# Kernel tuning notes

Measured on AMD Instinct MI355X. Metric: run time of the kernel, lower is better.

Reference implementation:

```python
import jax, jax.numpy as jnp
import numpy as np

NEG_INF = -1e30


def setup_inputs() -> dict:
    B, N, D = 512, 256, 256
    key = jax.random.key(0)
    ks = jax.random.split(key, 10)
    s = 1.0 / np.sqrt(D)
    return {
        "enc": jax.random.normal(ks[0], (B, N, D), dtype=jnp.float32),
        "init_token": jax.random.normal(ks[1], (D,), dtype=jnp.float32),
        "w_ih": jax.random.uniform(ks[2], (3 * D, D), minval=-s, maxval=s, dtype=jnp.float32),
        "w_hh": jax.random.uniform(ks[3], (3 * D, D), minval=-s, maxval=s, dtype=jnp.float32),
        "b_ih": jax.random.uniform(ks[4], (3 * D,), minval=-s, maxval=s, dtype=jnp.float32),
        "b_hh": jax.random.uniform(ks[5], (3 * D,), minval=-s, maxval=s, dtype=jnp.float32),
        "wq": jax.random.uniform(ks[6], (D, D), minval=-s, maxval=s, dtype=jnp.float32),
        "bq": jax.random.uniform(ks[7], (D,), minval=-s, maxval=s, dtype=jnp.float32),
        "wk": jax.random.uniform(ks[8], (D, D), minval=-s, maxval=s, dtype=jnp.float32),
        "bk": jax.random.uniform(ks[9], (D,), minval=-s, maxval=s, dtype=jnp.float32),
    }


def gru_cell(x, h, w_ih, w_hh, b_ih, b_hh):
    # torch.nn.GRUCell math; gates packed as [reset, update, new]
    gi = x @ w_ih.T + b_ih          # [B, 3D]
    gh = h @ w_hh.T + b_hh          # [B, 3D]
    D = h.shape[-1]
    i_r, i_z, i_n = gi[:, :D], gi[:, D:2 * D], gi[:, 2 * D:]
    h_r, h_z, h_n = gh[:, :D], gh[:, D:2 * D], gh[:, 2 * D:]
    r = jax.nn.sigmoid(i_r + h_r)
    z = jax.nn.sigmoid(i_z + h_z)
    n = jnp.tanh(i_n + r * h_n)
    return (1.0 - z) * n + z * h


def pointer_decode(enc, init_token, w_ih, w_hh, b_ih, b_hh, wq, bq, wk, bk):
    # Greedy decode (deterministic analogue of decode_type='greedy').
    B, N, D = enc.shape
    scale = 1.0 / np.sqrt(D)
    keys = enc @ wk.T + bk                         # [B, N, D]
    rows = jnp.arange(B)

    def step(carry, _):
        state, prev_embed, mask = carry
        state = gru_cell(prev_embed, state, w_ih, w_hh, b_ih, b_hh)   # [B, D]
        query = state @ wq.T + bq                                     # [B, D]
        logits = jnp.einsum('bd,bnd->bn', query, keys) * scale        # [B, N]
        logits = jnp.where(mask, logits, NEG_INF)
        logp = jax.nn.log_softmax(logits, axis=-1)                    # [B, N]
        probs = jnp.exp(logp)
        entropy = -jnp.sum(probs * jnp.where(mask, logp, 0.0), axis=-1)  # [B]
        idx = jnp.argmax(probs, axis=-1)                              # [B]
        step_logp = logp[rows, idx]                                   # [B]
        prev_embed = enc[rows, idx]                                   # [B, D]
        mask = mask.at[rows, idx].set(False)
        return (state, prev_embed, mask), (idx, step_logp, entropy)

    carry0 = (enc.mean(axis=1),
              jnp.broadcast_to(init_token, (B, D)),
              jnp.ones((B, N), dtype=bool))
    _, (tours, logps, ents) = jax.lax.scan(step, carry0, None, length=N)
    return tours.T, logps.T, ents.T  # each [B, N]


def reference(enc, init_token, w_ih, w_hh, b_ih, b_hh, wq, bq, wk, bk):
    return pointer_decode(enc, init_token, w_ih, w_hh, b_ih, b_hh, wq, bq, wk, bk)
```

## Files before the change

### kernel.cpp

```cpp
#include <hip/hip_runtime.h>

#define B_ 512
#define N_ 256
#define D_ 256
#define NEGINF (-1e30)
#define LN2_ 0.693147180559945309417232121458

#define PDX(c) ((c) + (((c) >> 6) << 1))

typedef float v4f __attribute__((ext_vector_type(4)));

__device__ __forceinline__ v4f ntload4(const v4f* p) {
  return __builtin_nontemporal_load(p);
}
__device__ __forceinline__ double ntload8(const double* p) {
  return __builtin_nontemporal_load(p);
}

__global__ void transpose_k(const float* __restrict__ in, float* __restrict__ out,
                            int R, int C) {
  __shared__ float tile[32][33];
  int rb = blockIdx.y * 32, cb = blockIdx.x * 32;
  int tx = threadIdx.x, ty = threadIdx.y;
  for (int i = ty; i < 32; i += 8) {
    int r = rb + i, c = cb + tx;
    if (r < R && c < C) tile[i][tx] = in[r * C + c];
  }
  __syncthreads();
  for (int i = ty; i < 32; i += 8) {
    int c = cb + i, r = rb + tx;
    if (r < R && c < C) out[c * R + r] = tile[tx][i];
  }
}

__global__ __launch_bounds__(256) void packW_k(const float* __restrict__ in,
                                               float* __restrict__ out) {
  int idx = blockIdx.x * 256 + threadIdx.x;
  int j = idx >> 6, c4 = idx & 63;
  int g = j >> 8, o = j & 255;
  int WV = o >> 5, S = c4 >> 5, k = c4 & 31, l = 2 * (o & 31) + S;
  ((v4f*)out)[((WV * 32 + k) * 3 + g) * 64 + l] = ((const v4f*)in)[idx];
}

__global__ __launch_bounds__(256) void wqk_k(const float* __restrict__ wk,
                                             const float* __restrict__ wq,
                                             const float* __restrict__ bq,
                                             double* __restrict__ WqkP,
                                             double* __restrict__ bqk) {
  int c = blockIdx.x, e = threadIdx.x;
  double acc = 0.0;
  for (int dd = 0; dd < 256; ++dd)
    acc += (double)wk[dd * 256 + c] * (double)wq[dd * 256 + e];
  int WV = c >> 5, l = 2 * (c & 31) + (e >> 7), k = (e & 127) >> 1, comp = e & 1;
  WqkP[(size_t)((WV * 64 + k) * 64 + l) * 2 + comp] = acc;
  if (e == 0) {
    double s = 0.0;
    for (int dd = 0; dd < 256; ++dd) s += (double)wk[dd * 256 + c] * (double)bq[dd];
    bqk[c] = s;
  }
}

__global__ __launch_bounds__(256) void encp_k(const float* __restrict__ enc,
                                              float* __restrict__ encP) {
  int b = blockIdx.y;
  int idx = blockIdx.x * 256 + threadIdx.x;
  int l = idx & 63, rest = idx >> 6;
  int k = rest & 31, WV = rest >> 5;
  int n = WV * 32 + (l >> 1), c4 = (l & 1) * 32 + k;
  ((v4f*)encP)[(size_t)b * 16384 + idx] =
      *(const v4f*)(enc + (size_t)b * 65536 + n * 256 + c4 * 4);
}

__global__ __launch_bounds__(768) void gi_k(const float* __restrict__ enc,
                                            const float* __restrict__ wihT,
                                            const float* __restrict__ b_ih,
                                            double* __restrict__ Gi) {
  int b = blockIdx.x, j = threadIdx.x;
  __shared__ float encS[32][256];
  const float* encB = enc + (size_t)b * 65536;
  double bias = (double)b_ih[j];
  for (int n0 = 0; n0 < 256; n0 += 32) {
    __syncthreads();
    for (int i = j; i < 2048; i += 768)
      ((float4*)encS)[i] = ((const float4*)(encB + n0 * 256))[i];
    __syncthreads();
    double acc[32];
#pragma unroll
    for (int jj = 0; jj < 32; ++jj) acc[jj] = bias;
    for (int c0 = 0; c0 < 256; c0 += 4) {
      double w0 = (double)wihT[(c0 + 0) * 768 + j];
      double w1 = (double)wihT[(c0 + 1) * 768 + j];
      double w2 = (double)wihT[(c0 + 2) * 768 + j];
      double w3 = (double)wihT[(c0 + 3) * 768 + j];
#pragma unroll
      for (int jj = 0; jj < 32; ++jj) {
        const float4 e = *(const float4*)&encS[jj][c0];
        acc[jj] += w0 * (double)e.x + w1 * (double)e.y + w2 * (double)e.z + w3 * (double)e.w;
      }
    }
#pragma unroll
    for (int jj = 0; jj < 32; ++jj)
      Gi[((size_t)b * 256 + n0 + jj) * 768 + j] = acc[jj];
  }
}

__global__ __launch_bounds__(768) void gi0_k(const float* __restrict__ w_ih,
                                             const float* __restrict__ b_ih,
                                             const float* __restrict__ init_token,
                                             double* __restrict__ gi0) {
  int j = threadIdx.x;
  __shared__ float xs[256];
  if (j < 256) xs[j] = init_token[j];
  __syncthreads();
  double acc = (double)b_ih[j];
  for (int c = 0; c < 256; ++c) acc += (double)w_ih[j * 256 + c] * (double)xs[c];
  gi0[j] = acc;
}

template <bool USE_GI>
__global__ __launch_bounds__(512, 4) void decode_k(
    const float* __restrict__ enc, const float* __restrict__ init_token,
    const float* __restrict__ b_ih, const float* __restrict__ b_hh,
    const float* __restrict__ wihP, const float* __restrict__ whhP,
    const double* __restrict__ WqkP, const double* __restrict__ bqk,
    const float* __restrict__ encP, const double* __restrict__ gi0,
    const double* __restrict__ Gi, float* __restrict__ out) {
  const int tid = threadIdx.x;
  const int WV = tid >> 6;
  const int LN = tid & 63;
  const int O = WV * 32 + (LN >> 1);
  const int S = LN & 1;
  const int b = blockIdx.x;
  const int OP = PDX(O);
  const int CB = S * 132;

  __shared__ alignas(16) double hS[2][264];
  __shared__ alignas(16) double xS[264];
  __shared__ alignas(16) double qs[264];
  __shared__ unsigned char maskS[N_];
  __shared__ double redA[8], redB[8], redC[8];
  __shared__ int redI[8];

  const float* encB = enc + (size_t)b * 65536;
  const v4f* eP = (const v4f*)encP + (size_t)b * 16384;
  const v4f* wh4 = (const v4f*)whhP;
  const v4f* wi4 = (const v4f*)wihP;
  const double2* Wp2 = (const double2*)WqkP;

  double giR[3];

  if (tid < 256) {
    maskS[tid] = 1;
    if (!USE_GI) xS[PDX(tid)] = (double)init_token[tid];
  }
  if (USE_GI) {
#pragma unroll
    for (int g = 0; g < 3; ++g) giR[g] = gi0[g * 256 + O];
  }
  {
    double p = 0.0;
    const float* e0 = encB + (size_t)(S * 128) * 256 + O;
#pragma unroll 4
    for (int n = 0; n < 128; ++n) p += (double)e0[n * 256];
    p += __shfl_xor(p, 1);
    if (S == 0) hS[0][OP] = p * (1.0 / 256.0);
  }
  __syncthreads();

  int cur = 0;
  for (int t = 0; t < N_; ++t) {
    const int nxt = cur ^ 1;
    double ghr = 0, ghz = 0, ghn = 0;
    double air = 0, aiz = 0, ain = 0;
#pragma unroll 4
    for (int k = 0; k < 32; ++k) {
      int wb = ((WV * 32 + k) * 3) * 64 + LN;
      v4f br = wh4[wb], bz = wh4[wb + 64], bn = wh4[wb + 128];
      const double* h = &hS[cur][CB + 4 * k + ((k >> 4) << 1)];
#pragma unroll
      for (int i = 0; i < 4; ++i) {
        ghr += (double)br[i] * h[i];
        ghz += (double)bz[i] * h[i];
        ghn += (double)bn[i] * h[i];
      }
      if (!USE_GI) {
        v4f ar = wi4[wb], az = wi4[wb + 64], an = wi4[wb + 128];
        const double* x = &xS[CB + 4 * k + ((k >> 4) << 1)];
#pragma unroll
        for (int i = 0; i < 4; ++i) {
          air += (double)ar[i] * x[i];
          aiz += (double)az[i] * x[i];
          ain += (double)an[i] * x[i];
        }
      }
    }
    ghr += __shfl_xor(ghr, 1);
    ghz += __shfl_xor(ghz, 1);
    ghn += __shfl_xor(ghn, 1);
    if (!USE_GI) {
      air += __shfl_xor(air, 1);
      aiz += __shfl_xor(aiz, 1);
      ain += __shfl_xor(ain, 1);
    }
    {
      double gir, giz, gin;
      if (USE_GI) {
        gir = giR[0]; giz = giR[1]; gin = giR[2];
      } else {
        gir = air + (double)b_ih[O];
        giz = aiz + (double)b_ih[256 + O];
        gin = ain + (double)b_ih[512 + O];
      }
      double hr_ = ghr + (double)b_hh[O];
      double hz_ = ghz + (double)b_hh[256 + O];
      double hn_ = ghn + (double)b_hh[512 + O];
      double rr = 1.0 / (1.0 + exp(-(gir + hr_)));
      double zz = 1.0 / (1.0 + exp(-(giz + hz_)));
      double nn = tanh(gin + rr * hn_);
      double hold = hS[cur][OP];
      double hnew = (1.0 - zz) * nn + zz * hold;
      if (S == 0) hS[nxt][OP] = hnew;
    }
    __syncthreads();

    {
      double q = 0;
#pragma unroll 8
      for (int k = 0; k < 64; ++k) {
        double2 wv = Wp2[(WV * 64 + k) * 64 + LN];
        const double* h = &hS[nxt][CB + 2 * k + ((k >> 5) << 1)];
        q += wv.x * h[0] + wv.y * h[1];
      }
      q += __shfl_xor(q, 1);
      if (S == 0) qs[OP] = q + bqk[O];
    }
    __syncthreads();

    {
      double p = 0;
#pragma unroll 8
      for (int k = 0; k < 32; ++k) {
        v4f e = ntload4(eP + (WV * 32 + k) * 64 + LN);
        const double* qa = &qs[CB + 4 * k + ((k >> 4) << 1)];
#pragma unroll
        for (int i = 0; i < 4; ++i) p += (double)e[i] * qa[i];
      }
      p += __shfl_xor(p, 1);
      double lgv = 0.0625 * p;
      if (!maskS[O]) lgv = NEGINF;
      double v = lgv;
      int idx = O;
#pragma unroll
      for (int off = 1; off < 64; off <<= 1) {
        double ov = __shfl_xor(v, off); int oi = __shfl_xor(idx, off);
        if (ov > v || (ov == v && oi < idx)) { v = ov; idx = oi; }
      }
      double e1 = exp(lgv - v);
      double s2 = e1 * (lgv - v);
#pragma unroll
      for (int off = 1; off < 64; off <<= 1) {
        e1 += __shfl_xor(e1, off);
        s2 += __shfl_xor(s2, off);
      }
      if (LN == 0) { redA[WV] = v; redI[WV] = idx; redB[WV] = e1; redC[WV] = s2; }
    }
    __syncthreads();

    if (tid < 8) {
      double mw = redA[tid];
      int iw = redI[tid];
      double s1w = redB[tid], s2w = redC[tid];
      double m = mw;
      int am = iw;
#pragma unroll
      for (int off = 1; off < 8; off <<= 1) {
        double om = __shfl_xor(m, off); int oi = __shfl_xor(am, off);
        if (om > m || (om == m && oi < am)) { m = om; am = oi; }
      }
      double sc = exp(mw - m);
      double S1 = s1w * sc;
      double S2 = (s2w + (mw - m) * s1w) * sc;
#pragma unroll
      for (int off = 1; off < 8; off <<= 1) {
        S1 += __shfl_xor(S1, off);
        S2 += __shfl_xor(S2, off);
      }
      if (tid == 0) {
        double lS = log(S1) - LN2_;
        size_t row = (size_t)b * N_;
        out[row + t] = (float)am;
        out[(size_t)B_ * N_ + row + t] = (float)(-lS);
        out[2 * (size_t)B_ * N_ + row + t] = (float)(lS - S2 / S1);
        maskS[am] = 0;
      }
    }
    {
      double bv = redA[0];
      int am = redI[0];
#pragma unroll
      for (int w = 1; w < 8; ++w) {
        double wv = redA[w]; int wi = redI[w];
        if (wv > bv || (wv == bv && wi < am)) { bv = wv; am = wi; }
      }
      if (USE_GI) {
        const double* gp = Gi + ((size_t)b * 256 + am) * 768;
        giR[0] = ntload8(gp + O);
        giR[1] = ntload8(gp + 256 + O);
        giR[2] = ntload8(gp + 512 + O);
      } else {
        if (tid < 256) {
          int j = tid, c4 = j >> 2;
          int vidx = ((am >> 5) * 32 + (c4 & 31)) * 64 + (2 * (am & 31) + (c4 >> 5));
          xS[PDX(j)] = (double)((const float*)eP)[vidx * 4 + (j & 3)];
        }
      }
    }
    __syncthreads();
    cur ^= 1;
  }
}

extern "C" void kernel_launch(void* const* d_in, const int* in_sizes, int n_in,
                              void* d_out, int out_size, void* d_ws, size_t ws_size,
                              hipStream_t stream) {
  const float* enc = (const float*)d_in[0];
  const float* init_token = (const float*)d_in[1];
  const float* w_ih = (const float*)d_in[2];
  const float* w_hh = (const float*)d_in[3];
  const float* b_ih = (const float*)d_in[4];
  const float* b_hh = (const float*)d_in[5];
  const float* wq = (const float*)d_in[6];
  const float* bq = (const float*)d_in[7];
  const float* wk = (const float*)d_in[8];
  const float* bk = (const float*)d_in[9];
  (void)bk;
  float* out = (float*)d_out;
  char* wsb = (char*)d_ws;

  float* wihP = (float*)(wsb + 0);
  float* whhP = (float*)(wsb + 786432);
  double* WqkP = (double*)(wsb + 1572864);
  double* bqk = (double*)(wsb + 2097152);
  double* gi0 = (double*)(wsb + 2099200);
  float* encP = (float*)(wsb + 2105344);
  float* wihT = (float*)(wsb + 136323072);
  double* Gi = (double*)(wsb + 137109504);
  const bool useGi = ws_size >= 942415872ull;

  hipLaunchKernelGGL(packW_k, dim3(192), dim3(256), 0, stream, w_ih, wihP);
  hipLaunchKernelGGL(packW_k, dim3(192), dim3(256), 0, stream, w_hh, whhP);
  hipLaunchKernelGGL(wqk_k, dim3(256), dim3(256), 0, stream, wk, wq, bq, WqkP, bqk);
  hipLaunchKernelGGL(encp_k, dim3(64, 512), dim3(256), 0, stream, enc, encP);
  hipLaunchKernelGGL(gi0_k, dim3(1), dim3(768), 0, stream, w_ih, b_ih, init_token, gi0);
  if (useGi) {
    hipLaunchKernelGGL(transpose_k, dim3(8, 24), dim3(32, 8), 0, stream, w_ih, wihT, 768, 256);
    hipLaunchKernelGGL(gi_k, dim3(512), dim3(768), 0, stream, enc, wihT, b_ih, Gi);
    hipLaunchKernelGGL(decode_k<true>, dim3(B_), dim3(512), 0, stream, enc, init_token,
                       b_ih, b_hh, wihP, whhP, WqkP, bqk, encP, gi0, Gi, out);
  } else {
    hipLaunchKernelGGL(decode_k<false>, dim3(B_), dim3(512), 0, stream, enc, init_token,
                       b_ih, b_hh, wihP, whhP, WqkP, bqk, encP, gi0, Gi, out);
  }
}
```

Baseline: 17.04 ms.

## Keep each block's encoder rows resident in registers across decode steps

Result: slower. 27.52 ms (+61.5%).

```diff
diff --git a/kernel.cpp b/kernel.cpp
--- a/kernel.cpp
+++ b/kernel.cpp
@@ -10,9 +10,6 @@
 
 typedef float v4f __attribute__((ext_vector_type(4)));
 
-__device__ __forceinline__ v4f ntload4(const v4f* p) {
-  return __builtin_nontemporal_load(p);
-}
 __device__ __forceinline__ double ntload8(const double* p) {
   return __builtin_nontemporal_load(p);
 }
@@ -60,17 +57,6 @@
   }
 }
 
-__global__ __launch_bounds__(256) void encp_k(const float* __restrict__ enc,
-                                              float* __restrict__ encP) {
-  int b = blockIdx.y;
-  int idx = blockIdx.x * 256 + threadIdx.x;
-  int l = idx & 63, rest = idx >> 6;
-  int k = rest & 31, WV = rest >> 5;
-  int n = WV * 32 + (l >> 1), c4 = (l & 1) * 32 + k;
-  ((v4f*)encP)[(size_t)b * 16384 + idx] =
-      *(const v4f*)(enc + (size_t)b * 65536 + n * 256 + c4 * 4);
-}
-
 __global__ __launch_bounds__(768) void gi_k(const float* __restrict__ enc,
                                             const float* __restrict__ wihT,
                                             const float* __restrict__ b_ih,
@@ -118,13 +104,13 @@
 }
 
 template <bool USE_GI>
-__global__ __launch_bounds__(512, 4) void decode_k(
+__global__ __launch_bounds__(512, 2) void decode_k(
     const float* __restrict__ enc, const float* __restrict__ init_token,
     const float* __restrict__ b_ih, const float* __restrict__ b_hh,
     const float* __restrict__ wihP, const float* __restrict__ whhP,
     const double* __restrict__ WqkP, const double* __restrict__ bqk,
-    const float* __restrict__ encP, const double* __restrict__ gi0,
-    const double* __restrict__ Gi, float* __restrict__ out) {
+    const double* __restrict__ gi0, const double* __restrict__ Gi,
+    float* __restrict__ out) {
   const int tid = threadIdx.x;
   const int WV = tid >> 6;
   const int LN = tid & 63;
@@ -142,10 +128,16 @@
   __shared__ int redI[8];
 
   const float* encB = enc + (size_t)b * 65536;
-  const v4f* eP = (const v4f*)encP + (size_t)b * 16384;
   const v4f* wh4 = (const v4f*)whhP;
   const v4f* wi4 = (const v4f*)wihP;
   const double2* Wp2 = (const double2*)WqkP;
+
+  v4f encR[32];
+  {
+    const float* encRow = encB + O * 256 + S * 128;
+#pragma unroll
+    for (int k = 0; k < 32; ++k) encR[k] = *(const v4f*)(encRow + 4 * k);
+  }
 
   double giR[3];
 
@@ -238,10 +230,10 @@
 
     {
       double p = 0;
-#pragma unroll 8
+#pragma unroll
       for (int k = 0; k < 32; ++k) {
-        v4f e = ntload4(eP + (WV * 32 + k) * 64 + LN);
         const double* qa = &qs[CB + 4 * k + ((k >> 4) << 1)];
+        v4f e = encR[k];
 #pragma unroll
         for (int i = 0; i < 4; ++i) p += (double)e[i] * qa[i];
       }
@@ -308,10 +300,13 @@
         giR[1] = ntload8(gp + 256 + O);
         giR[2] = ntload8(gp + 512 + O);
       } else {
-        if (tid < 256) {
-          int j = tid, c4 = j >> 2;
-          int vidx = ((am >> 5) * 32 + (c4 & 31)) * 64 + (2 * (am & 31) + (c4 >> 5));
-          xS[PDX(j)] = (double)((const float*)eP)[vidx * 4 + (j & 3)];
+        if (O == am) {
+#pragma unroll
+          for (int k = 0; k < 32; ++k) {
+#pragma unroll
+            for (int i = 0; i < 4; ++i)
+              xS[PDX(S * 128 + 4 * k + i)] = (double)encR[k][i];
+          }
         }
       }
     }
@@ -342,23 +337,21 @@
   double* WqkP = (double*)(wsb + 1572864);
   double* bqk = (double*)(wsb + 2097152);
   double* gi0 = (double*)(wsb + 2099200);
-  float* encP = (float*)(wsb + 2105344);
-  float* wihT = (float*)(wsb + 136323072);
-  double* Gi = (double*)(wsb + 137109504);
-  const bool useGi = ws_size >= 942415872ull;
+  float* wihT = (float*)(wsb + 2105344);
+  double* Gi = (double*)(wsb + 2891776);
+  const bool useGi = ws_size >= 808198144ull;
 
   hipLaunchKernelGGL(packW_k, dim3(192), dim3(256), 0, stream, w_ih, wihP);
   hipLaunchKernelGGL(packW_k, dim3(192), dim3(256), 0, stream, w_hh, whhP);
   hipLaunchKernelGGL(wqk_k, dim3(256), dim3(256), 0, stream, wk, wq, bq, WqkP, bqk);
-  hipLaunchKernelGGL(encp_k, dim3(64, 512), dim3(256), 0, stream, enc, encP);
   hipLaunchKernelGGL(gi0_k, dim3(1), dim3(768), 0, stream, w_ih, b_ih, init_token, gi0);
   if (useGi) {
     hipLaunchKernelGGL(transpose_k, dim3(8, 24), dim3(32, 8), 0, stream, w_ih, wihT, 768, 256);
     hipLaunchKernelGGL(gi_k, dim3(512), dim3(768), 0, stream, enc, wihT, b_ih, Gi);
     hipLaunchKernelGGL(decode_k<true>, dim3(B_), dim3(512), 0, stream, enc, init_token,
-                       b_ih, b_hh, wihP, whhP, WqkP, bqk, encP, gi0, Gi, out);
+                       b_ih, b_hh, wihP, whhP, WqkP, bqk, gi0, Gi, out);
   } else {
     hipLaunchKernelGGL(decode_k<false>, dim3(B_), dim3(512), 0, stream, enc, init_token,
-                       b_ih, b_hh, wihP, whhP, WqkP, bqk, encP, gi0, Gi, out);
-  }
-}
+                       b_ih, b_hh, wihP, whhP, WqkP, bqk, gi0, Gi, out);
+  }
+}
```
